# Kernel tuning notes

Measured on AMD Instinct MI355X. Metric: run time of the kernel, lower is better.

Reference implementation:

```python
import jax, jax.numpy as jnp
import numpy as np
from jax import lax

B, C, S = 32, 1, 65536
H = 32  # hidden_size


def setup_inputs() -> dict:
    key = jax.random.key(0)
    ks = jax.random.split(key, 7)
    scale = 1.0 / np.sqrt(H)  # torch LSTM/Linear default init range
    x = jax.random.normal(ks[0], (B, C, S), dtype=jnp.float32)
    W_ih = jax.random.uniform(ks[1], (4 * H, C), minval=-scale, maxval=scale, dtype=jnp.float32)
    W_hh = jax.random.uniform(ks[2], (4 * H, H), minval=-scale, maxval=scale, dtype=jnp.float32)
    b_ih = jax.random.uniform(ks[3], (4 * H,), minval=-scale, maxval=scale, dtype=jnp.float32)
    b_hh = jax.random.uniform(ks[4], (4 * H,), minval=-scale, maxval=scale, dtype=jnp.float32)
    W_lin = jax.random.uniform(ks[5], (1, H), minval=-scale, maxval=scale, dtype=jnp.float32)
    b_lin = jax.random.uniform(ks[6], (1,), minval=-scale, maxval=scale, dtype=jnp.float32)
    return {"x": x, "W_ih": W_ih, "W_hh": W_hh, "b_ih": b_ih, "b_hh": b_hh,
            "W_lin": W_lin, "b_lin": b_lin}


def _lstm_head(x, W_ih, W_hh, b_ih, b_hh, W_lin, b_lin):
    # x: (B, 1, S) -> (S, B, 1), matching x.permute(2, 0, 1)
    xs = jnp.transpose(x, (2, 0, 1))
    b = x.shape[0]
    # Precompute input contribution to gates for all timesteps: (S, B, 4H)
    pre = jnp.einsum('sbi,gi->sbg', xs, W_ih) + (b_ih + b_hh)

    def step(carry, px):
        h, c = carry
        gates = px + h @ W_hh.T  # (B, 4H), gate order i, f, g, o (torch)
        i, f, g, o = jnp.split(gates, 4, axis=-1)
        c = jax.nn.sigmoid(f) * c + jax.nn.sigmoid(i) * jnp.tanh(g)
        h = jax.nn.sigmoid(o) * jnp.tanh(c)
        return (h, c), h

    h0 = jnp.zeros((b, H), dtype=x.dtype)
    (_, _), hs = lax.scan(step, (h0, h0), pre)  # hs: (S, B, H)
    y = jnp.tanh(hs @ W_lin.T + b_lin)  # linear head + tanh, (S, B, 1)
    return jnp.transpose(y, (1, 2, 0))  # (B, 1, S)


def reference(x, W_ih, W_hh, b_ih, b_hh, W_lin, b_lin):
    return _lstm_head(x, W_ih, W_hh, b_ih, b_hh, W_lin, b_lin)
```

## Files before the change

### kernel.cpp

```cpp
#include <hip/hip_runtime.h>

#define HID     32
#define SLEN    65536
#define NB      32
#define UNROLL  32
#define NBLK    (SLEN / UNROLL)
#define RSTRIDE 36

typedef float    f32x2 __attribute__((ext_vector_type(2)));
typedef float    f32x4 __attribute__((ext_vector_type(4)));
typedef unsigned u32x2 __attribute__((ext_vector_type(2)));

__device__ __forceinline__ float fast_sigmoid(float x) {
    float e = __builtin_amdgcn_exp2f(-1.4426950408889634f * x);
    return __builtin_amdgcn_rcpf(1.0f + e);
}
__device__ __forceinline__ float fast_tanh(float x) {
    float e = __builtin_amdgcn_exp2f(2.8853900817779268f * x);
    return 1.0f - 2.0f * __builtin_amdgcn_rcpf(1.0f + e);
}

#if __has_builtin(__builtin_elementwise_fma)
__device__ __forceinline__ f32x2 pkfma(f32x2 a, f32x2 b, f32x2 c) {
    return __builtin_elementwise_fma(a, b, c);
}
#else
__device__ __forceinline__ f32x2 pkfma(f32x2 a, f32x2 b, f32x2 c) {
    f32x2 r; r.x = fmaf(a.x, b.x, c.x); r.y = fmaf(a.y, b.y, c.y); return r;
}
#endif

#if __has_builtin(__builtin_amdgcn_permlane32_swap)
#define HAVE_PERMLANE_SWAP 1
__device__ __forceinline__ void half_exchange(float g, bool , float& low_own, float& up_own) {
    u32x2 r = __builtin_amdgcn_permlane32_swap(__float_as_uint(g), __float_as_uint(g), false, false);
    low_own = __uint_as_float(r.x);
    up_own  = __uint_as_float(r.y);
}
#else
#define HAVE_PERMLANE_SWAP 0
__device__ __forceinline__ void half_exchange(float g, bool lo, float& low_own, float& up_own) {
    const float p = __shfl_xor(g, 32, 64);
    low_own = lo ? g : p;
    up_own  = lo ? p : g;
}
#endif

__global__ __launch_bounds__(64, 1) void lstm_scan_kernel(
    const float* __restrict__ x,
    const float* __restrict__ W_ih,
    const float* __restrict__ W_hh,
    const float* __restrict__ b_ih,
    const float* __restrict__ b_hh,
    const float* __restrict__ W_lin,
    const float* __restrict__ b_lin,
    float* __restrict__ out)
{
    const int  b    = blockIdx.x;
    const int  lane = threadIdx.x;
    const int  k    = lane & 31;
    const bool lo   = (lane < 32);

    __shared__ __align__(16) float hlds[32 * RSTRIDE];

    const f32x2* wr0 = (const f32x2*)(W_hh + lane * HID);
    const f32x2* wr1 = (const f32x2*)(W_hh + (lane + 64) * HID);
    f32x2 w0p[16], w1p[16];
    #pragma unroll
    for (int j = 0; j < 16; ++j) { w0p[j] = wr0[j]; w1p[j] = wr1[j]; }
    const float bias0 = b_ih[lane]      + b_hh[lane];
    const float bias1 = b_ih[lane + 64] + b_hh[lane + 64];
    const float wih0  = W_ih[lane];
    const float wih1  = W_ih[lane + 64];
    const float blin  = b_lin[0];

    const int ys = lane >> 1;
    const int yr = (lane & 1) << 4;
    const f32x4* wlv = (const f32x4*)(W_lin + yr);
    f32x4 wl0 = wlv[0], wl1 = wlv[1], wl2 = wlv[2], wl3 = wlv[3];

    if (lo) hlds[31 * RSTRIDE + k] = 0.0f;

    float c = 0.0f;
    const float* __restrict__ xb = x   + (size_t)b * SLEN;
    float* __restrict__       ob = out + (size_t)b * SLEN;

    f32x4 xc[8];
    {
        const f32x4* xg = (const f32x4*)xb;
        #pragma unroll
        for (int q = 0; q < 8; ++q) xc[q] = xg[q];
    }

    for (int blk = 0; blk < NBLK; ++blk) {
        const int nb_ = (blk + 1 < NBLK) ? (blk + 1) : blk;
        const f32x4* xg = (const f32x4*)(xb + nb_ * UNROLL);
        f32x4 xn0 = xg[0], xn1 = xg[1], xn2 = xg[2], xn3 = xg[3];
        f32x4 xn4 = xg[4], xn5 = xg[5], xn6 = xg[6], xn7 = xg[7];

        #pragma unroll
        for (int u = 0; u < UNROLL; ++u) {
            const int rs = (u + 31) & 31;
            const f32x4* hp = (const f32x4*)(hlds + rs * RSTRIDE);
            f32x4 hq[8];
            #pragma unroll
            for (int j = 0; j < 8; ++j) hq[j] = hp[j];

            const float xt = xc[u >> 2][u & 3];

            f32x2 a0 = { fmaf(xt, wih0, bias0), 0.0f }, a1 = { 0.0f, 0.0f };
            f32x2 b0 = { fmaf(xt, wih1, bias1), 0.0f }, b1 = { 0.0f, 0.0f };
            #pragma unroll
            for (int j = 0; j < 8; ++j) {
                const f32x2 l2 = __builtin_shufflevector(hq[j], hq[j], 0, 1);
                const f32x2 h2 = __builtin_shufflevector(hq[j], hq[j], 2, 3);
                a0 = pkfma(l2, w0p[2 * j],     a0);
                a1 = pkfma(h2, w0p[2 * j + 1], a1);
                b0 = pkfma(l2, w1p[2 * j],     b0);
                b1 = pkfma(h2, w1p[2 * j + 1], b1);
            }
            const f32x2 sa = a0 + a1;
            const f32x2 sb = b0 + b1;
            const float g0 = sa.x + sa.y;
            const float g1 = sb.x + sb.y;

            float gi, gf, gg, go;
            half_exchange(g0, lo, gi, gf);
            half_exchange(g1, lo, gg, go);

            c = fmaf(fast_sigmoid(gf), c, fast_sigmoid(gi) * fast_tanh(gg));
            const float h = fast_sigmoid(go) * fast_tanh(c);
            if (lo) hlds[u * RSTRIDE + k] = h;
        }

        {
            const f32x4* yp = (const f32x4*)(hlds + ys * RSTRIDE + yr);
            f32x4 h0 = yp[0], h1 = yp[1], h2 = yp[2], h3 = yp[3];
            float acc;
            acc = h0.x * wl0.x;
            acc = fmaf(h0.y, wl0.y, acc); acc = fmaf(h0.z, wl0.z, acc); acc = fmaf(h0.w, wl0.w, acc);
            acc = fmaf(h1.x, wl1.x, acc); acc = fmaf(h1.y, wl1.y, acc);
            acc = fmaf(h1.z, wl1.z, acc); acc = fmaf(h1.w, wl1.w, acc);
            acc = fmaf(h2.x, wl2.x, acc); acc = fmaf(h2.y, wl2.y, acc);
            acc = fmaf(h2.z, wl2.z, acc); acc = fmaf(h2.w, wl2.w, acc);
            acc = fmaf(h3.x, wl3.x, acc); acc = fmaf(h3.y, wl3.y, acc);
            acc = fmaf(h3.z, wl3.z, acc); acc = fmaf(h3.w, wl3.w, acc);
            acc += __shfl_xor(acc, 1, 64);
            if ((lane & 1) == 0) ob[blk * UNROLL + ys] = fast_tanh(acc + blin);
        }

        xc[0] = xn0; xc[1] = xn1; xc[2] = xn2; xc[3] = xn3;
        xc[4] = xn4; xc[5] = xn5; xc[6] = xn6; xc[7] = xn7;
    }
}

extern "C" void kernel_launch(void* const* d_in, const int* in_sizes, int n_in,
                              void* d_out, int out_size, void* d_ws, size_t ws_size,
                              hipStream_t stream) {
    (void)d_ws; (void)ws_size; (void)in_sizes; (void)n_in; (void)out_size;
    const float* x     = (const float*)d_in[0];
    const float* W_ih  = (const float*)d_in[1];
    const float* W_hh  = (const float*)d_in[2];
    const float* b_ih  = (const float*)d_in[3];
    const float* b_hh  = (const float*)d_in[4];
    const float* W_lin = (const float*)d_in[5];
    const float* b_lin = (const float*)d_in[6];
    float* out = (float*)d_out;

    hipLaunchKernelGGL(lstm_scan_kernel, dim3(NB), dim3(64), 0, stream,
                       x, W_ih, W_hh, b_ih, b_hh, W_lin, b_lin, out);
}
```

Baseline: 13.30 ms.

## Broadcast hidden state via readlane instead of LDS round-trip per step

The recurrent matvec now broadcasts each hidden element with v_readlane from the owning lane, replacing the per-step LDS store/load of the full hidden vector. The LDS copy is kept only for the output head. The block size grows to 64 steps so every lane loads one x value and writes one output per block. This removes the LDS write-read latency from the serial dependency chain, at the cost of 32 readlanes per step (scalar-register transfers with VALU-to-SGPR hazards) and scalar FMAs in place of packed FMAs.

Result: slower. 18.93 ms (+42.4%).

```diff
diff --git a/kernel.cpp b/kernel.cpp
--- a/kernel.cpp
+++ b/kernel.cpp
@@ -3,11 +3,10 @@
 #define HID     32
 #define SLEN    65536
 #define NB      32
-#define UNROLL  32
-#define NBLK    (SLEN / UNROLL)
+#define BSTEP   64
+#define NBLK    (SLEN / BSTEP)
 #define RSTRIDE 36
 
-typedef float    f32x2 __attribute__((ext_vector_type(2)));
 typedef float    f32x4 __attribute__((ext_vector_type(4)));
 typedef unsigned u32x2 __attribute__((ext_vector_type(2)));
 
@@ -20,25 +19,17 @@
     return 1.0f - 2.0f * __builtin_amdgcn_rcpf(1.0f + e);
 }
 
-#if __has_builtin(__builtin_elementwise_fma)
-__device__ __forceinline__ f32x2 pkfma(f32x2 a, f32x2 b, f32x2 c) {
-    return __builtin_elementwise_fma(a, b, c);
+__device__ __forceinline__ float rl(float v, int j) {
+    return __uint_as_float(__builtin_amdgcn_readlane(__float_as_uint(v), j));
 }
-#else
-__device__ __forceinline__ f32x2 pkfma(f32x2 a, f32x2 b, f32x2 c) {
-    f32x2 r; r.x = fmaf(a.x, b.x, c.x); r.y = fmaf(a.y, b.y, c.y); return r;
-}
-#endif
 
 #if __has_builtin(__builtin_amdgcn_permlane32_swap)
-#define HAVE_PERMLANE_SWAP 1
-__device__ __forceinline__ void half_exchange(float g, bool , float& low_own, float& up_own) {
+__device__ __forceinline__ void half_exchange(float g, bool, float& low_own, float& up_own) {
     u32x2 r = __builtin_amdgcn_permlane32_swap(__float_as_uint(g), __float_as_uint(g), false, false);
     low_own = __uint_as_float(r.x);
     up_own  = __uint_as_float(r.y);
 }
 #else
-#define HAVE_PERMLANE_SWAP 0
 __device__ __forceinline__ void half_exchange(float g, bool lo, float& low_own, float& up_own) {
     const float p = __shfl_xor(g, 32, 64);
     low_own = lo ? g : p;
@@ -61,96 +52,86 @@
     const int  k    = lane & 31;
     const bool lo   = (lane < 32);
 
-    __shared__ __align__(16) float hlds[32 * RSTRIDE];
+    __shared__ __align__(16) float hlds[BSTEP * RSTRIDE];
 
-    const f32x2* wr0 = (const f32x2*)(W_hh + lane * HID);
-    const f32x2* wr1 = (const f32x2*)(W_hh + (lane + 64) * HID);
-    f32x2 w0p[16], w1p[16];
-    #pragma unroll
-    for (int j = 0; j < 16; ++j) { w0p[j] = wr0[j]; w1p[j] = wr1[j]; }
+    float w0[HID], w1[HID];
+    {
+        const f32x4* r0 = (const f32x4*)(W_hh + lane * HID);
+        const f32x4* r1 = (const f32x4*)(W_hh + (lane + 64) * HID);
+        #pragma unroll
+        for (int q = 0; q < 8; ++q) {
+            f32x4 v0 = r0[q], v1 = r1[q];
+            w0[4*q+0] = v0.x; w0[4*q+1] = v0.y; w0[4*q+2] = v0.z; w0[4*q+3] = v0.w;
+            w1[4*q+0] = v1.x; w1[4*q+1] = v1.y; w1[4*q+2] = v1.z; w1[4*q+3] = v1.w;
+        }
+    }
     const float bias0 = b_ih[lane]      + b_hh[lane];
     const float bias1 = b_ih[lane + 64] + b_hh[lane + 64];
     const float wih0  = W_ih[lane];
     const float wih1  = W_ih[lane + 64];
     const float blin  = b_lin[0];
 
-    const int ys = lane >> 1;
-    const int yr = (lane & 1) << 4;
-    const f32x4* wlv = (const f32x4*)(W_lin + yr);
-    f32x4 wl0 = wlv[0], wl1 = wlv[1], wl2 = wlv[2], wl3 = wlv[3];
+    float wls[HID];
+    #pragma unroll
+    for (int j = 0; j < HID; ++j) wls[j] = W_lin[j];
 
-    if (lo) hlds[31 * RSTRIDE + k] = 0.0f;
-
-    float c = 0.0f;
+    float hcur = 0.0f, ccur = 0.0f;
     const float* __restrict__ xb = x   + (size_t)b * SLEN;
     float* __restrict__       ob = out + (size_t)b * SLEN;
 
-    f32x4 xc[8];
-    {
-        const f32x4* xg = (const f32x4*)xb;
-        #pragma unroll
-        for (int q = 0; q < 8; ++q) xc[q] = xg[q];
-    }
+    float xcur = xb[lane];
 
+    #pragma unroll 1
     for (int blk = 0; blk < NBLK; ++blk) {
         const int nb_ = (blk + 1 < NBLK) ? (blk + 1) : blk;
-        const f32x4* xg = (const f32x4*)(xb + nb_ * UNROLL);
-        f32x4 xn0 = xg[0], xn1 = xg[1], xn2 = xg[2], xn3 = xg[3];
-        f32x4 xn4 = xg[4], xn5 = xg[5], xn6 = xg[6], xn7 = xg[7];
+        float xnext = xb[nb_ * BSTEP + lane];
 
-        #pragma unroll
-        for (int u = 0; u < UNROLL; ++u) {
-            const int rs = (u + 31) & 31;
-            const f32x4* hp = (const f32x4*)(hlds + rs * RSTRIDE);
-            f32x4 hq[8];
+        #pragma unroll 1
+        for (int i = 0; i < BSTEP / 4; ++i) {
             #pragma unroll
-            for (int j = 0; j < 8; ++j) hq[j] = hp[j];
+            for (int c4 = 0; c4 < 4; ++c4) {
+                const int u  = 4 * i + c4;
+                const float xt = rl(xcur, u);
 
-            const float xt = xc[u >> 2][u & 3];
+                float A0 = fmaf(xt, wih0, bias0), A1 = 0.0f;
+                float B0 = fmaf(xt, wih1, bias1), B1 = 0.0f;
+                #pragma unroll
+                for (int j = 0; j < HID; j += 2) {
+                    const float hj0 = rl(hcur, j);
+                    const float hj1 = rl(hcur, j + 1);
+                    A0 = fmaf(hj0, w0[j],     A0);
+                    A1 = fmaf(hj1, w0[j + 1], A1);
+                    B0 = fmaf(hj0, w1[j],     B0);
+                    B1 = fmaf(hj1, w1[j + 1], B1);
+                }
+                const float g0 = A0 + A1;
+                const float g1 = B0 + B1;
 
-            f32x2 a0 = { fmaf(xt, wih0, bias0), 0.0f }, a1 = { 0.0f, 0.0f };
-            f32x2 b0 = { fmaf(xt, wih1, bias1), 0.0f }, b1 = { 0.0f, 0.0f };
-            #pragma unroll
-            for (int j = 0; j < 8; ++j) {
-                const f32x2 l2 = __builtin_shufflevector(hq[j], hq[j], 0, 1);
-                const f32x2 h2 = __builtin_shufflevector(hq[j], hq[j], 2, 3);
-                a0 = pkfma(l2, w0p[2 * j],     a0);
-                a1 = pkfma(h2, w0p[2 * j + 1], a1);
-                b0 = pkfma(l2, w1p[2 * j],     b0);
-                b1 = pkfma(h2, w1p[2 * j + 1], b1);
+                float gi, gf, gg, go;
+                half_exchange(g0, lo, gi, gf);
+                half_exchange(g1, lo, gg, go);
+
+                ccur = fmaf(fast_sigmoid(gf), ccur, fast_sigmoid(gi) * fast_tanh(gg));
+                hcur = fast_sigmoid(go) * fast_tanh(ccur);
+                if (lo) hlds[u * RSTRIDE + k] = hcur;
             }
-            const f32x2 sa = a0 + a1;
-            const f32x2 sb = b0 + b1;
-            const float g0 = sa.x + sa.y;
-            const float g1 = sb.x + sb.y;
-
-            float gi, gf, gg, go;
-            half_exchange(g0, lo, gi, gf);
-            half_exchange(g1, lo, gg, go);
-
-            c = fmaf(fast_sigmoid(gf), c, fast_sigmoid(gi) * fast_tanh(gg));
-            const float h = fast_sigmoid(go) * fast_tanh(c);
-            if (lo) hlds[u * RSTRIDE + k] = h;
         }
 
         {
-            const f32x4* yp = (const f32x4*)(hlds + ys * RSTRIDE + yr);
-            f32x4 h0 = yp[0], h1 = yp[1], h2 = yp[2], h3 = yp[3];
-            float acc;
-            acc = h0.x * wl0.x;
-            acc = fmaf(h0.y, wl0.y, acc); acc = fmaf(h0.z, wl0.z, acc); acc = fmaf(h0.w, wl0.w, acc);
-            acc = fmaf(h1.x, wl1.x, acc); acc = fmaf(h1.y, wl1.y, acc);
-            acc = fmaf(h1.z, wl1.z, acc); acc = fmaf(h1.w, wl1.w, acc);
-            acc = fmaf(h2.x, wl2.x, acc); acc = fmaf(h2.y, wl2.y, acc);
-            acc = fmaf(h2.z, wl2.z, acc); acc = fmaf(h2.w, wl2.w, acc);
-            acc = fmaf(h3.x, wl3.x, acc); acc = fmaf(h3.y, wl3.y, acc);
-            acc = fmaf(h3.z, wl3.z, acc); acc = fmaf(h3.w, wl3.w, acc);
-            acc += __shfl_xor(acc, 1, 64);
-            if ((lane & 1) == 0) ob[blk * UNROLL + ys] = fast_tanh(acc + blin);
+            const f32x4* h4 = (const f32x4*)(hlds + lane * RSTRIDE);
+            float acc = blin;
+            #pragma unroll
+            for (int q = 0; q < 8; ++q) {
+                const f32x4 hv = h4[q];
+                acc = fmaf(hv.x, wls[4*q+0], acc);
+                acc = fmaf(hv.y, wls[4*q+1], acc);
+                acc = fmaf(hv.z, wls[4*q+2], acc);
+                acc = fmaf(hv.w, wls[4*q+3], acc);
+            }
+            ob[blk * BSTEP + lane] = fast_tanh(acc);
         }
 
-        xc[0] = xn0; xc[1] = xn1; xc[2] = xn2; xc[3] = xn3;
-        xc[4] = xn4; xc[5] = xn5; xc[6] = xn6; xc[7] = xn7;
+        xcur = xnext;
     }
 }
 
```
